# Kernel tuning notes

Hardware: AMD Instinct MI355X
Metric: run time of the kernel (lower is better)

## Reference

```python
import jax, jax.numpy as jnp
import numpy as np

R = 128          # voxel grid resolution
B = 2            # batch size
NPB = 250_000    # active voxels per batch item
N = B * NPB      # total active voxels
C_IN = 32        # in_nchannel
C0 = 32          # enc_ch[0] = out_nchannel
C1 = 32          # enc_ch[1]
EPS = 1e-5


def _build_neighbor_maps():
    """Build Minkowski-style kernel maps: for each kernel offset k and output
    voxel n, nmap[k, n] = index of the input voxel at coord+offset, or -1."""
    rng = np.random.default_rng(0)
    keys_list = []
    for b in range(B):
        flat = rng.choice(R ** 3, NPB, replace=False).astype(np.int64)
        keys_list.append(b * (R ** 3) + np.sort(flat))
    keys = np.concatenate(keys_list)  # globally sorted (batch-major)
    local = keys % (R ** 3)
    bidx = keys // (R ** 3)
    x = local // (R * R)
    y = (local // R) % R
    z = local % R

    def make(offsets):
        nmap = np.full((len(offsets), N), -1, dtype=np.int32)
        for k, (dx, dy, dz) in enumerate(offsets):
            nx, ny, nz = x + dx, y + dy, z + dz
            valid = (nx >= 0) & (nx < R) & (ny >= 0) & (ny < R) & (nz >= 0) & (nz < R)
            nkey = bidx * (R ** 3) + nx * R * R + ny * R + nz
            pos = np.searchsorted(keys, nkey)
            pos_c = np.clip(pos, 0, N - 1)
            valid &= keys[pos_c] == nkey
            nmap[k] = np.where(valid, pos_c, -1)
        return nmap

    off3 = [(dx, dy, dz) for dx in (-1, 0, 1) for dy in (-1, 0, 1) for dz in (-1, 0, 1)]
    off2 = [(dx, dy, dz) for dx in (0, 1) for dy in (0, 1) for dz in (0, 1)]
    return jnp.asarray(make(off3)), jnp.asarray(make(off2))


def setup_inputs() -> dict:
    key = jax.random.key(0)
    ks = jax.random.split(key, 8)
    nmap3, nmap2 = _build_neighbor_maps()
    s3_in = 1.0 / np.sqrt(27 * C_IN)
    s2 = 1.0 / np.sqrt(8 * C0)
    s3 = 1.0 / np.sqrt(27 * C1)
    return {
        "feats": jax.random.normal(ks[0], (N, C_IN), jnp.float32),
        "W1": jax.random.normal(ks[1], (27, C_IN, C0), jnp.float32) * s3_in,
        "g1": jnp.ones((C0,), jnp.float32),
        "b1": jnp.zeros((C0,), jnp.float32),
        "W2": jax.random.normal(ks[2], (8, C0, C1), jnp.float32) * s2,
        "g2": jnp.ones((C1,), jnp.float32),
        "b2": jnp.zeros((C1,), jnp.float32),
        "W3": jax.random.normal(ks[3], (27, C1, C1), jnp.float32) * s3,
        "g3": jnp.ones((C1,), jnp.float32),
        "b3": jnp.zeros((C1,), jnp.float32),
        "nmap3": nmap3,
        "nmap2": nmap2,
    }


def sparse_conv(feats, nmap, W):
    """MinkowskiConvolution (no bias): gather neighbors per kernel offset,
    GEMM with that offset's weight, accumulate. Loop is over the fixed,
    small kernel volume (8 or 27), not over data."""
    out = jnp.zeros((feats.shape[0], W.shape[-1]), feats.dtype)
    for k in range(W.shape[0]):
        idx = nmap[k]
        g = jnp.where((idx >= 0)[:, None], feats[jnp.maximum(idx, 0)], 0.0)
        out = out + g @ W[k]
    return out


def bn_elu(x, gamma, beta):
    # MinkowskiBatchNorm over all active voxels (training-mode stats) + ELU
    mean = jnp.mean(x, axis=0)
    var = jnp.var(x, axis=0)
    xn = (x - mean) * jax.lax.rsqrt(var + EPS)
    return jax.nn.elu(xn * gamma + beta)


def reference(feats, W1, g1, b1, W2, g2, b2, W3, g3, b3, nmap3, nmap2):
    # enc_block_s1: conv k=3 s=1 -> BN -> ELU
    h = bn_elu(sparse_conv(feats, nmap3, W1), g1, b1)
    # enc_block_s1s2: conv k=2 s=1 -> BN -> ELU -> conv k=3 -> BN -> ELU
    h = bn_elu(sparse_conv(h, nmap2, W2), g2, b2)
    h = bn_elu(sparse_conv(h, nmap3, W3), g3, b3)
    return h
```

## Files before the change

### kernel.cpp

```cpp
#include <hip/hip_runtime.h>


typedef short shortx8 __attribute__((ext_vector_type(8)));
typedef float floatx4 __attribute__((ext_vector_type(4)));

__device__ __forceinline__ float bf2f(unsigned short h) {
    unsigned u = ((unsigned)h) << 16;
    return __builtin_bit_cast(float, u);
}
__device__ __forceinline__ unsigned short f2bf(float f) {
    unsigned u = __builtin_bit_cast(unsigned, f);
    return (unsigned short)((u + 0x7fffu + ((u >> 16) & 1u)) >> 16);
}

__device__ __forceinline__ void gl_lds16(const void* g, void* l) {
    __builtin_amdgcn_global_load_lds(
        (const __attribute__((address_space(1))) unsigned*)g,
        (__attribute__((address_space(3))) unsigned*)l, 16, 0, 0);
}

__global__ void detect_dtype(const unsigned* __restrict__ g1, int* __restrict__ flag) {
    if (threadIdx.x == 0) *flag = (g1[0] == 0x3F800000u) ? 1 : 0;
}

__global__ __launch_bounds__(256) void prep_w_all(
    const void* __restrict__ W1_, const void* __restrict__ W2_,
    const void* __restrict__ W3_, unsigned short* __restrict__ Wg,
    const int* __restrict__ flag)
{
    int o = blockIdx.x * 256 + threadIdx.x;
    if (o >= 62 * 1024) return;
    const void* W; int lo;
    if (o < 27648)      { W = W1_; lo = o; }
    else if (o < 35840) { W = W2_; lo = o - 27648; }
    else                { W = W3_; lo = o - 35840; }
    int j = lo & 7, lane = (lo >> 3) & 63, f = (lo >> 9) & 1, k = lo >> 10;
    int col = lane & 15, quad = lane >> 4;
    int src = k * 1024 + (quad * 8 + j) * 32 + f * 16 + col;
    unsigned short v = *flag ? f2bf(((const float*)W)[src])
                             : ((const unsigned short*)W)[src];
    Wg[o] = v;
}

__global__ __launch_bounds__(256) void normalize_feats(
    const void* __restrict__ in_, unsigned short* __restrict__ out,
    int total, const int* __restrict__ flag)
{
    if (!*flag) return;
    int i = (blockIdx.x * 256 + threadIdx.x) * 8;
    if (i >= total) return;
    const float* in = (const float*)in_;
    floatx4 a = *(const floatx4*)(in + i);
    floatx4 b = *(const floatx4*)(in + i + 4);
    unsigned o[4];
    o[0] = (unsigned)f2bf(a[0]) | ((unsigned)f2bf(a[1]) << 16);
    o[1] = (unsigned)f2bf(a[2]) | ((unsigned)f2bf(a[3]) << 16);
    o[2] = (unsigned)f2bf(b[0]) | ((unsigned)f2bf(b[1]) << 16);
    o[3] = (unsigned)f2bf(b[2]) | ((unsigned)f2bf(b[3]) << 16);
    uint4 ov = {o[0], o[1], o[2], o[3]};
    *(uint4*)(out + i) = ov;
}

template <int KV>
__global__ __launch_bounds__(512, 4) void conv_stats(
    const unsigned short* __restrict__ feats,
    const unsigned short* __restrict__ feats_alt,
    const unsigned short* __restrict__ Wg,
    const int* __restrict__ nmap,
    unsigned short* __restrict__ xout,
    float* __restrict__ stat,
    int N,
    const int* __restrict__ flagA)
{
    constexpr int CH  = (KV >= 9) ? 9 : KV;
    constexpr int NCH = KV / CH;
    static_assert(KV % CH == 0, "chunking assumes CH | KV");
    constexpr int BUFB = CH * 4096;

    __shared__ __align__(16) char smem[2 * BUFB + 2048];
    float* red = (float*)(smem + 2 * BUFB);

    const int tid  = threadIdx.x;
    const int lane = tid & 63, wave = tid >> 6;
    const int col  = lane & 15, quad = lane >> 4;
    const int row0 = blockIdx.x * 512;
    const int m0   = row0 + wave * 64;
    const unsigned short* A = (*flagA) ? feats_alt : feats;

    auto stage = [&](int c) {
        const int kc = c * CH;
        char* buf = smem + (c & 1) * BUFB;
        for (int s = wave; s < CH * 4; s += 8) {
            int ki = s >> 2, part = s & 3;
            if (part < 2) {
                int r4 = row0 + part * 256 + lane * 4;
                if (r4 > N - 4) r4 = N - 4;
                gl_lds16(nmap + (size_t)(kc + ki) * N + r4,
                         buf + ki * 2048 + part * 1024);
            } else {
                gl_lds16(Wg + (kc + ki) * 1024 + (part - 2) * 512 + lane * 8,
                         buf + CH * 2048 + ki * 2048 + (part - 2) * 1024);
            }
        }
    };

    floatx4 accA[4], accB[4];
#pragma unroll
    for (int t = 0; t < 4; ++t) {
        accA[t] = {0.f, 0.f, 0.f, 0.f};
        accB[t] = {0.f, 0.f, 0.f, 0.f};
    }

    int rown[4];
#pragma unroll
    for (int t = 0; t < 4; ++t) rown[t] = m0 + t * 16 + col;

    stage(0);
    __syncthreads();

    for (int c = 0; c < NCH; ++c) {
        if (c + 1 < NCH) stage(c + 1);
        const int* nsl = (const int*)(smem + (c & 1) * BUFB);
        const unsigned short* wsl =
            (const unsigned short*)(smem + (c & 1) * BUFB + CH * 2048);

        shortx8 ring[2][4];
#pragma unroll
        for (int p = 0; p < 2; ++p) {
#pragma unroll
            for (int t = 0; t < 4; ++t) {
                int id = (rown[t] < N) ? nsl[p * 512 + wave * 64 + t * 16 + col] : -1;
                shortx8 a = {0, 0, 0, 0, 0, 0, 0, 0};
                if (id >= 0) a = *(const shortx8*)(A + (size_t)id * 32 + quad * 8);
                ring[p][t] = a;
            }
        }

#pragma unroll
        for (int kk = 0; kk < CH; ++kk) {
            shortx8 at[4];
#pragma unroll
            for (int t = 0; t < 4; ++t) at[t] = ring[kk & 1][t];

            if (kk + 2 < CH) {
#pragma unroll
                for (int t = 0; t < 4; ++t) {
                    int id = (rown[t] < N)
                                 ? nsl[(kk + 2) * 512 + wave * 64 + t * 16 + col]
                                 : -1;
                    shortx8 a = {0, 0, 0, 0, 0, 0, 0, 0};
                    if (id >= 0) a = *(const shortx8*)(A + (size_t)id * 32 + quad * 8);
                    ring[kk & 1][t] = a;
                }
            }

            shortx8 b0 = *(const shortx8*)(wsl + kk * 1024 + lane * 8);
            shortx8 b1 = *(const shortx8*)(wsl + kk * 1024 + 512 + lane * 8);
#pragma unroll
            for (int t = 0; t < 4; ++t) {
                accA[t] = __builtin_amdgcn_mfma_f32_16x16x32_bf16(at[t], b0, accA[t], 0, 0, 0);
                accB[t] = __builtin_amdgcn_mfma_f32_16x16x32_bf16(at[t], b1, accB[t], 0, 0, 0);
            }
            __builtin_amdgcn_sched_barrier(0);
        }
        __syncthreads();
    }

#pragma unroll
    for (int t = 0; t < 4; ++t) {
        int rbase = m0 + t * 16 + quad * 4;
#pragma unroll
        for (int r = 0; r < 4; ++r) {
            int row = rbase + r;
            if (row < N) {
                xout[row * 32 + col]      = f2bf(accA[t][r]);
                xout[row * 32 + col + 16] = f2bf(accB[t][r]);
            }
        }
    }

    float s0 = 0.f, s1 = 0.f, q0 = 0.f, q1 = 0.f;
#pragma unroll
    for (int t = 0; t < 4; ++t) {
#pragma unroll
        for (int r = 0; r < 4; ++r) {
            s0 += accA[t][r]; q0 += accA[t][r] * accA[t][r];
            s1 += accB[t][r]; q1 += accB[t][r] * accB[t][r];
        }
    }
    s0 += __shfl_xor(s0, 16); s0 += __shfl_xor(s0, 32);
    s1 += __shfl_xor(s1, 16); s1 += __shfl_xor(s1, 32);
    q0 += __shfl_xor(q0, 16); q0 += __shfl_xor(q0, 32);
    q1 += __shfl_xor(q1, 16); q1 += __shfl_xor(q1, 32);

    if (lane < 16) {
        float* rw = red + wave * 64;
        rw[col]      = s0;
        rw[col + 16] = s1;
        rw[col + 32] = q0;
        rw[col + 48] = q1;
    }
    __syncthreads();
    if (tid < 64) {
        float v = 0.f;
#pragma unroll
        for (int w = 0; w < 8; ++w) v += red[tid + w * 64];
        atomicAdd(stat + tid, v);
    }
}

__global__ __launch_bounds__(256) void bn_elu_apply(
    const unsigned short* __restrict__ x,
    const float* __restrict__ stat,
    const void* __restrict__ g_,
    const void* __restrict__ b_,
    void* __restrict__ out_,
    int total, int N, int finalout,
    const int* __restrict__ flag)
{
    __shared__ float ps[64];
    int tid = threadIdx.x;
    if (tid < 32) {
        int f = *flag;
        float gv = f ? ((const float*)g_)[tid] : bf2f(((const unsigned short*)g_)[tid]);
        float bv = f ? ((const float*)b_)[tid] : bf2f(((const unsigned short*)b_)[tid]);
        float invN = 1.0f / (float)N;
        float mean = stat[tid] * invN;
        float var  = fmaxf(stat[32 + tid] * invN - mean * mean, 0.0f);
        float sc   = gv * rsqrtf(var + 1e-5f);
        ps[tid]      = sc;
        ps[32 + tid] = bv - mean * sc;
    }
    __syncthreads();

    int i = (blockIdx.x * 256 + tid) * 8;
    if (i >= total) return;

    uint4 v = *(const uint4*)(x + i);
    int c0 = i & 31;
    unsigned w[4] = {v.x, v.y, v.z, v.w};
    float y[8];
#pragma unroll
    for (int j = 0; j < 4; ++j) {
        int c = c0 + 2 * j;
        float f0 = bf2f((unsigned short)(w[j] & 0xffffu));
        float f1 = bf2f((unsigned short)(w[j] >> 16));
        float y0 = f0 * ps[c]     + ps[32 + c];
        float y1 = f1 * ps[c + 1] + ps[32 + c + 1];
        y[2*j]     = y0 > 0.f ? y0 : (__expf(y0) - 1.f);
        y[2*j + 1] = y1 > 0.f ? y1 : (__expf(y1) - 1.f);
    }

    if (finalout && *flag) {
        float* o = (float*)out_ + i;
        floatx4 o0 = {y[0], y[1], y[2], y[3]};
        floatx4 o1 = {y[4], y[5], y[6], y[7]};
        *(floatx4*)o = o0;
        *(floatx4*)(o + 4) = o1;
    } else {
        unsigned o[4];
#pragma unroll
        for (int j = 0; j < 4; ++j)
            o[j] = (unsigned)f2bf(y[2*j]) | ((unsigned)f2bf(y[2*j + 1]) << 16);
        uint4 ov = {o[0], o[1], o[2], o[3]};
        *(uint4*)((unsigned short*)out_ + i) = ov;
    }
}

extern "C" void kernel_launch(void* const* d_in, const int* in_sizes, int n_in,
                              void* d_out, int out_size, void* d_ws, size_t ws_size,
                              hipStream_t stream)
{
    const void* feats = d_in[0];
    const void* W1    = d_in[1];
    const void* g1    = d_in[2];
    const void* b1    = d_in[3];
    const void* W2    = d_in[4];
    const void* g2    = d_in[5];
    const void* b2    = d_in[6];
    const void* W3    = d_in[7];
    const void* g3    = d_in[8];
    const void* b3    = d_in[9];
    const int* nmap3  = (const int*)d_in[10];
    const int* nmap2  = (const int*)d_in[11];

    const int N = in_sizes[0] / 32;
    const int total = N * 32;

    char* ws = (char*)d_ws;
    float* stat0 = (float*)(ws);
    float* stat1 = (float*)(ws + 256);
    float* stat2 = (float*)(ws + 512);
    int*   flagD = (int*)(ws + 768);
    unsigned short* Wg  = (unsigned short*)(ws + 4096);
    unsigned short* Wg1 = Wg;
    unsigned short* Wg2 = Wg + 27648;
    unsigned short* Wg3 = Wg + 35840;
    unsigned short* xbuf = (unsigned short*)(ws + 131072);
    unsigned short* hbuf = (unsigned short*)d_out;

    hipMemsetAsync(d_ws, 0, 1024, stream);
    detect_dtype<<<1, 64, 0, stream>>>((const unsigned*)g1, flagD);

    prep_w_all<<<(62 * 1024 + 255) / 256, 256, 0, stream>>>(W1, W2, W3, Wg, flagD);
    normalize_feats<<<(total / 8 + 255) / 256, 256, 0, stream>>>(feats, hbuf, total, flagD);

    const int cblocks = (N + 511) / 512;
    const int ablocks = (total / 8 + 255) / 256;

    conv_stats<27><<<cblocks, 512, 0, stream>>>(
        (const unsigned short*)feats, hbuf, Wg1, nmap3, xbuf, stat0, N, flagD);
    bn_elu_apply<<<ablocks, 256, 0, stream>>>(xbuf, stat0, g1, b1, hbuf, total, N, 0, flagD);

    conv_stats<8><<<cblocks, 512, 0, stream>>>(
        hbuf, hbuf, Wg2, nmap2, xbuf, stat1, N, flagD);
    bn_elu_apply<<<ablocks, 256, 0, stream>>>(xbuf, stat1, g2, b2, hbuf, total, N, 0, flagD);

    conv_stats<27><<<cblocks, 512, 0, stream>>>(
        hbuf, hbuf, Wg3, nmap3, xbuf, stat2, N, flagD);
    bn_elu_apply<<<ablocks, 256, 0, stream>>>(xbuf, stat2, g3, b3, d_out, total, N, 1, flagD);
}
```

Before: 354.4 us.

## Prefetch neighbor indices into registers and stage all weights in LDS once

The chunked double-buffered LDS staging of neighbor-map indices and weights is removed. Each thread now loads its own nmap indices straight from global memory with nontemporal loads, four offsets ahead, and gathers features three offsets deep into a register ring. All KV weight slices are copied to LDS once up front, so the per-chunk syncthreads go away. Invalid neighbors read from a zeroed row in workspace instead of taking a branch. This uses more registers for the deeper prefetch queues, which may lower occupancy.

After: 377.1 us. +6.4%, slower.

```diff
diff --git a/kernel.cpp b/kernel.cpp
--- a/kernel.cpp
+++ b/kernel.cpp
@@ -67,42 +67,29 @@
     const unsigned short* __restrict__ feats_alt,
     const unsigned short* __restrict__ Wg,
     const int* __restrict__ nmap,
+    const unsigned short* __restrict__ zrow,
     unsigned short* __restrict__ xout,
     float* __restrict__ stat,
     int N,
     const int* __restrict__ flagA)
 {
-    constexpr int CH  = (KV >= 9) ? 9 : KV;
-    constexpr int NCH = KV / CH;
-    static_assert(KV % CH == 0, "chunking assumes CH | KV");
-    constexpr int BUFB = CH * 4096;
-
-    __shared__ __align__(16) char smem[2 * BUFB + 2048];
-    float* red = (float*)(smem + 2 * BUFB);
+    __shared__ __align__(16) char smem[KV * 2048 + 2048];
+    float* red = (float*)(smem + KV * 2048);
 
     const int tid  = threadIdx.x;
     const int lane = tid & 63, wave = tid >> 6;
     const int col  = lane & 15, quad = lane >> 4;
-    const int row0 = blockIdx.x * 512;
-    const int m0   = row0 + wave * 64;
+    const int m0   = blockIdx.x * 512 + wave * 64;
     const unsigned short* A = (*flagA) ? feats_alt : feats;
 
-    auto stage = [&](int c) {
-        const int kc = c * CH;
-        char* buf = smem + (c & 1) * BUFB;
-        for (int s = wave; s < CH * 4; s += 8) {
-            int ki = s >> 2, part = s & 3;
-            if (part < 2) {
-                int r4 = row0 + part * 256 + lane * 4;
-                if (r4 > N - 4) r4 = N - 4;
-                gl_lds16(nmap + (size_t)(kc + ki) * N + r4,
-                         buf + ki * 2048 + part * 1024);
-            } else {
-                gl_lds16(Wg + (kc + ki) * 1024 + (part - 2) * 512 + lane * 8,
-                         buf + CH * 2048 + ki * 2048 + (part - 2) * 1024);
-            }
-        }
-    };
+    int rown[4], rcl[4];
+    bool ok[4];
+#pragma unroll
+    for (int t = 0; t < 4; ++t) {
+        rown[t] = m0 + t * 16 + col;
+        ok[t]   = rown[t] < N;
+        rcl[t]  = ok[t] ? rown[t] : (N - 1);
+    }
 
     floatx4 accA[4], accB[4];
 #pragma unroll
@@ -111,59 +98,45 @@
         accB[t] = {0.f, 0.f, 0.f, 0.f};
     }
 
-    int rown[4];
-#pragma unroll
-    for (int t = 0; t < 4; ++t) rown[t] = m0 + t * 16 + col;
-
-    stage(0);
+    int idxq[4][4];
+    shortx8 ring[3][4];
+
+    auto IDX = [&](int k) {
+#pragma unroll
+        for (int t = 0; t < 4; ++t) {
+            int id = __builtin_nontemporal_load(nmap + (size_t)k * N + rcl[t]);
+            idxq[k & 3][t] = ok[t] ? id : -1;
+        }
+    };
+    auto GAT = [&](int k) {
+#pragma unroll
+        for (int t = 0; t < 4; ++t) {
+            int id = idxq[k & 3][t];
+            const unsigned short* src = (id >= 0) ? (A + (size_t)id * 32) : zrow;
+            ring[k % 3][t] = *(const shortx8*)(src + quad * 8);
+        }
+    };
+
+    IDX(0); IDX(1); IDX(2); IDX(3);
+    for (int s = wave; s < KV * 2; s += 8)
+        gl_lds16(Wg + s * 512 + lane * 8, smem + s * 1024);
+    GAT(0); GAT(1);
     __syncthreads();
 
-    for (int c = 0; c < NCH; ++c) {
-        if (c + 1 < NCH) stage(c + 1);
-        const int* nsl = (const int*)(smem + (c & 1) * BUFB);
-        const unsigned short* wsl =
-            (const unsigned short*)(smem + (c & 1) * BUFB + CH * 2048);
-
-        shortx8 ring[2][4];
-#pragma unroll
-        for (int p = 0; p < 2; ++p) {
-#pragma unroll
-            for (int t = 0; t < 4; ++t) {
-                int id = (rown[t] < N) ? nsl[p * 512 + wave * 64 + t * 16 + col] : -1;
-                shortx8 a = {0, 0, 0, 0, 0, 0, 0, 0};
-                if (id >= 0) a = *(const shortx8*)(A + (size_t)id * 32 + quad * 8);
-                ring[p][t] = a;
-            }
-        }
-
-#pragma unroll
-        for (int kk = 0; kk < CH; ++kk) {
-            shortx8 at[4];
-#pragma unroll
-            for (int t = 0; t < 4; ++t) at[t] = ring[kk & 1][t];
-
-            if (kk + 2 < CH) {
-#pragma unroll
-                for (int t = 0; t < 4; ++t) {
-                    int id = (rown[t] < N)
-                                 ? nsl[(kk + 2) * 512 + wave * 64 + t * 16 + col]
-                                 : -1;
-                    shortx8 a = {0, 0, 0, 0, 0, 0, 0, 0};
-                    if (id >= 0) a = *(const shortx8*)(A + (size_t)id * 32 + quad * 8);
-                    ring[kk & 1][t] = a;
-                }
-            }
-
-            shortx8 b0 = *(const shortx8*)(wsl + kk * 1024 + lane * 8);
-            shortx8 b1 = *(const shortx8*)(wsl + kk * 1024 + 512 + lane * 8);
-#pragma unroll
-            for (int t = 0; t < 4; ++t) {
-                accA[t] = __builtin_amdgcn_mfma_f32_16x16x32_bf16(at[t], b0, accA[t], 0, 0, 0);
-                accB[t] = __builtin_amdgcn_mfma_f32_16x16x32_bf16(at[t], b1, accB[t], 0, 0, 0);
-            }
-            __builtin_amdgcn_sched_barrier(0);
-        }
-        __syncthreads();
+#pragma unroll
+    for (int k = 0; k < KV; ++k) {
+        if (k + 4 < KV) IDX(k + 4);
+        if (k + 2 < KV) GAT(k + 2);
+
+        const unsigned short* wk = (const unsigned short*)(smem + k * 2048);
+        shortx8 b0 = *(const shortx8*)(wk + lane * 8);
+        shortx8 b1 = *(const shortx8*)(wk + 512 + lane * 8);
+#pragma unroll
+        for (int t = 0; t < 4; ++t) {
+            accA[t] = __builtin_amdgcn_mfma_f32_16x16x32_bf16(ring[k % 3][t], b0, accA[t], 0, 0, 0);
+            accB[t] = __builtin_amdgcn_mfma_f32_16x16x32_bf16(ring[k % 3][t], b1, accB[t], 0, 0, 0);
+        }
+        __builtin_amdgcn_sched_barrier(0);
     }
 
 #pragma unroll
@@ -292,6 +265,7 @@
     float* stat1 = (float*)(ws + 256);
     float* stat2 = (float*)(ws + 512);
     int*   flagD = (int*)(ws + 768);
+    const unsigned short* zrow = (const unsigned short*)(ws + 1024);
     unsigned short* Wg  = (unsigned short*)(ws + 4096);
     unsigned short* Wg1 = Wg;
     unsigned short* Wg2 = Wg + 27648;
@@ -299,7 +273,7 @@
     unsigned short* xbuf = (unsigned short*)(ws + 131072);
     unsigned short* hbuf = (unsigned short*)d_out;
 
-    hipMemsetAsync(d_ws, 0, 1024, stream);
+    hipMemsetAsync(d_ws, 0, 2048, stream);
     detect_dtype<<<1, 64, 0, stream>>>((const unsigned*)g1, flagD);
 
     prep_w_all<<<(62 * 1024 + 255) / 256, 256, 0, stream>>>(W1, W2, W3, Wg, flagD);
@@ -309,14 +283,14 @@
     const int ablocks = (total / 8 + 255) / 256;
 
     conv_stats<27><<<cblocks, 512, 0, stream>>>(
-        (const unsigned short*)feats, hbuf, Wg1, nmap3, xbuf, stat0, N, flagD);
+        (const unsigned short*)feats, hbuf, Wg1, nmap3, zrow, xbuf, stat0, N, flagD);
     bn_elu_apply<<<ablocks, 256, 0, stream>>>(xbuf, stat0, g1, b1, hbuf, total, N, 0, flagD);
 
     conv_stats<8><<<cblocks, 512, 0, stream>>>(
-        hbuf, hbuf, Wg2, nmap2, xbuf, stat1, N, flagD);
+        hbuf, hbuf, Wg2, nmap2, zrow, xbuf, stat1, N, flagD);
     bn_elu_apply<<<ablocks, 256, 0, stream>>>(xbuf, stat1, g2, b2, hbuf, total, N, 0, flagD);
 
     conv_stats<27><<<cblocks, 512, 0, stream>>>(
-        hbuf, hbuf, Wg3, nmap3, xbuf, stat2, N, flagD);
+        hbuf, hbuf, Wg3, nmap3, zrow, xbuf, stat2, N, flagD);
     bn_elu_apply<<<ablocks, 256, 0, stream>>>(xbuf, stat2, g3, b3, d_out, total, N, 1, flagD);
 }
```

## Fuse all stages into one persistent kernel with software grid barriers

Applied to the files above, without the earlier changes.

Replaces the nine separate launches (dtype detect, weight prep, feature conversion, three conv+stats and three BN+ELU passes) with a single persistent kernel of 512 blocks. Phases are separated by an atomic-counter grid barrier, and each phase loops over tiles or elements with a grid stride. This removes launch gaps and inter-kernel idle time. In exchange, the fixed grid size may lower occupancy during the gather-heavy conv phases and adds barrier spin cost. It also relies on all blocks being co-resident.

Result: slower. 1.071 ms (+202.3%).

```diff
diff --git a/kernel.cpp b/kernel.cpp
--- a/kernel.cpp
+++ b/kernel.cpp
@@ -3,6 +3,9 @@
 
 typedef short shortx8 __attribute__((ext_vector_type(8)));
 typedef float floatx4 __attribute__((ext_vector_type(4)));
+
+constexpr int GRID_B = 512;
+constexpr int TPB    = 512;
 
 __device__ __forceinline__ float bf2f(unsigned short h) {
     unsigned u = ((unsigned)h) << 16;
@@ -19,252 +22,275 @@
         (__attribute__((address_space(3))) unsigned*)l, 16, 0, 0);
 }
 
-__global__ void detect_dtype(const unsigned* __restrict__ g1, int* __restrict__ flag) {
-    if (threadIdx.x == 0) *flag = (g1[0] == 0x3F800000u) ? 1 : 0;
-}
-
-__global__ __launch_bounds__(256) void prep_w_all(
-    const void* __restrict__ W1_, const void* __restrict__ W2_,
-    const void* __restrict__ W3_, unsigned short* __restrict__ Wg,
-    const int* __restrict__ flag)
-{
-    int o = blockIdx.x * 256 + threadIdx.x;
-    if (o >= 62 * 1024) return;
-    const void* W; int lo;
-    if (o < 27648)      { W = W1_; lo = o; }
-    else if (o < 35840) { W = W2_; lo = o - 27648; }
-    else                { W = W3_; lo = o - 35840; }
-    int j = lo & 7, lane = (lo >> 3) & 63, f = (lo >> 9) & 1, k = lo >> 10;
-    int col = lane & 15, quad = lane >> 4;
-    int src = k * 1024 + (quad * 8 + j) * 32 + f * 16 + col;
-    unsigned short v = *flag ? f2bf(((const float*)W)[src])
-                             : ((const unsigned short*)W)[src];
-    Wg[o] = v;
-}
-
-__global__ __launch_bounds__(256) void normalize_feats(
-    const void* __restrict__ in_, unsigned short* __restrict__ out,
-    int total, const int* __restrict__ flag)
-{
-    if (!*flag) return;
-    int i = (blockIdx.x * 256 + threadIdx.x) * 8;
-    if (i >= total) return;
-    const float* in = (const float*)in_;
-    floatx4 a = *(const floatx4*)(in + i);
-    floatx4 b = *(const floatx4*)(in + i + 4);
-    unsigned o[4];
-    o[0] = (unsigned)f2bf(a[0]) | ((unsigned)f2bf(a[1]) << 16);
-    o[1] = (unsigned)f2bf(a[2]) | ((unsigned)f2bf(a[3]) << 16);
-    o[2] = (unsigned)f2bf(b[0]) | ((unsigned)f2bf(b[1]) << 16);
-    o[3] = (unsigned)f2bf(b[2]) | ((unsigned)f2bf(b[3]) << 16);
-    uint4 ov = {o[0], o[1], o[2], o[3]};
-    *(uint4*)(out + i) = ov;
+__device__ __forceinline__ void gridbar(unsigned* cnt, unsigned* gen) {
+    __syncthreads();
+    if (threadIdx.x == 0) {
+        __threadfence();
+        unsigned g = __hip_atomic_load(gen, __ATOMIC_RELAXED, __HIP_MEMORY_SCOPE_AGENT);
+        unsigned a = __hip_atomic_fetch_add(cnt, 1u, __ATOMIC_ACQ_REL, __HIP_MEMORY_SCOPE_AGENT);
+        if (a == GRID_B - 1) {
+            __hip_atomic_store(cnt, 0u, __ATOMIC_RELAXED, __HIP_MEMORY_SCOPE_AGENT);
+            __hip_atomic_store(gen, g + 1u, __ATOMIC_RELEASE, __HIP_MEMORY_SCOPE_AGENT);
+        } else {
+            while (__hip_atomic_load(gen, __ATOMIC_ACQUIRE, __HIP_MEMORY_SCOPE_AGENT) == g)
+                __builtin_amdgcn_s_sleep(8);
+        }
+        __threadfence();
+    }
+    __syncthreads();
 }
 
 template <int KV>
-__global__ __launch_bounds__(512, 4) void conv_stats(
-    const unsigned short* __restrict__ feats,
-    const unsigned short* __restrict__ feats_alt,
-    const unsigned short* __restrict__ Wg,
-    const int* __restrict__ nmap,
-    unsigned short* __restrict__ xout,
-    float* __restrict__ stat,
-    int N,
-    const int* __restrict__ flagA)
+__device__ void conv_phase(char* smem,
+    const unsigned short* A, const unsigned short* Wg,
+    const int* nmap, unsigned short* xout, float* stat,
+    int N, int ntiles)
 {
     constexpr int CH  = (KV >= 9) ? 9 : KV;
     constexpr int NCH = KV / CH;
-    static_assert(KV % CH == 0, "chunking assumes CH | KV");
     constexpr int BUFB = CH * 4096;
-
-    __shared__ __align__(16) char smem[2 * BUFB + 2048];
     float* red = (float*)(smem + 2 * BUFB);
 
     const int tid  = threadIdx.x;
     const int lane = tid & 63, wave = tid >> 6;
     const int col  = lane & 15, quad = lane >> 4;
-    const int row0 = blockIdx.x * 512;
-    const int m0   = row0 + wave * 64;
-    const unsigned short* A = (*flagA) ? feats_alt : feats;
-
-    auto stage = [&](int c) {
-        const int kc = c * CH;
-        char* buf = smem + (c & 1) * BUFB;
-        for (int s = wave; s < CH * 4; s += 8) {
-            int ki = s >> 2, part = s & 3;
-            if (part < 2) {
-                int r4 = row0 + part * 256 + lane * 4;
-                if (r4 > N - 4) r4 = N - 4;
-                gl_lds16(nmap + (size_t)(kc + ki) * N + r4,
-                         buf + ki * 2048 + part * 1024);
-            } else {
-                gl_lds16(Wg + (kc + ki) * 1024 + (part - 2) * 512 + lane * 8,
-                         buf + CH * 2048 + ki * 2048 + (part - 2) * 1024);
-            }
-        }
-    };
-
-    floatx4 accA[4], accB[4];
-#pragma unroll
-    for (int t = 0; t < 4; ++t) {
-        accA[t] = {0.f, 0.f, 0.f, 0.f};
-        accB[t] = {0.f, 0.f, 0.f, 0.f};
-    }
-
-    int rown[4];
-#pragma unroll
-    for (int t = 0; t < 4; ++t) rown[t] = m0 + t * 16 + col;
-
-    stage(0);
-    __syncthreads();
-
-    for (int c = 0; c < NCH; ++c) {
-        if (c + 1 < NCH) stage(c + 1);
-        const int* nsl = (const int*)(smem + (c & 1) * BUFB);
-        const unsigned short* wsl =
-            (const unsigned short*)(smem + (c & 1) * BUFB + CH * 2048);
-
-        shortx8 ring[2][4];
-#pragma unroll
-        for (int p = 0; p < 2; ++p) {
-#pragma unroll
-            for (int t = 0; t < 4; ++t) {
-                int id = (rown[t] < N) ? nsl[p * 512 + wave * 64 + t * 16 + col] : -1;
-                shortx8 a = {0, 0, 0, 0, 0, 0, 0, 0};
-                if (id >= 0) a = *(const shortx8*)(A + (size_t)id * 32 + quad * 8);
-                ring[p][t] = a;
-            }
-        }
-
-#pragma unroll
-        for (int kk = 0; kk < CH; ++kk) {
-            shortx8 at[4];
-#pragma unroll
-            for (int t = 0; t < 4; ++t) at[t] = ring[kk & 1][t];
-
-            if (kk + 2 < CH) {
+
+    for (int tile = blockIdx.x; tile < ntiles; tile += GRID_B) {
+        const int row0 = tile * 512;
+        const int m0   = row0 + wave * 64;
+
+        auto stage = [&](int c) {
+            const int kc = c * CH;
+            char* buf = smem + (c & 1) * BUFB;
+            for (int s = wave; s < CH * 4; s += 8) {
+                int ki = s >> 2, part = s & 3;
+                if (part < 2) {
+                    int r4 = row0 + part * 256 + lane * 4;
+                    if (r4 > N - 4) r4 = N - 4;
+                    gl_lds16(nmap + (size_t)(kc + ki) * N + r4,
+                             buf + ki * 2048 + part * 1024);
+                } else {
+                    gl_lds16(Wg + (kc + ki) * 1024 + (part - 2) * 512 + lane * 8,
+                             buf + CH * 2048 + ki * 2048 + (part - 2) * 1024);
+                }
+            }
+        };
+
+        floatx4 accA[4], accB[4];
+#pragma unroll
+        for (int t = 0; t < 4; ++t) {
+            accA[t] = {0.f, 0.f, 0.f, 0.f};
+            accB[t] = {0.f, 0.f, 0.f, 0.f};
+        }
+
+        int rown[4];
+#pragma unroll
+        for (int t = 0; t < 4; ++t) rown[t] = m0 + t * 16 + col;
+
+        stage(0);
+        __syncthreads();
+
+        for (int c = 0; c < NCH; ++c) {
+            if (c + 1 < NCH) stage(c + 1);
+            const int* nsl = (const int*)(smem + (c & 1) * BUFB);
+            const unsigned short* wsl =
+                (const unsigned short*)(smem + (c & 1) * BUFB + CH * 2048);
+
+            shortx8 ring[2][4];
+#pragma unroll
+            for (int p = 0; p < 2; ++p) {
 #pragma unroll
                 for (int t = 0; t < 4; ++t) {
-                    int id = (rown[t] < N)
-                                 ? nsl[(kk + 2) * 512 + wave * 64 + t * 16 + col]
-                                 : -1;
+                    int id = (rown[t] < N) ? nsl[p * 512 + wave * 64 + t * 16 + col] : -1;
                     shortx8 a = {0, 0, 0, 0, 0, 0, 0, 0};
                     if (id >= 0) a = *(const shortx8*)(A + (size_t)id * 32 + quad * 8);
-                    ring[kk & 1][t] = a;
-                }
-            }
-
-            shortx8 b0 = *(const shortx8*)(wsl + kk * 1024 + lane * 8);
-            shortx8 b1 = *(const shortx8*)(wsl + kk * 1024 + 512 + lane * 8);
-#pragma unroll
-            for (int t = 0; t < 4; ++t) {
-                accA[t] = __builtin_amdgcn_mfma_f32_16x16x32_bf16(at[t], b0, accA[t], 0, 0, 0);
-                accB[t] = __builtin_amdgcn_mfma_f32_16x16x32_bf16(at[t], b1, accB[t], 0, 0, 0);
-            }
-            __builtin_amdgcn_sched_barrier(0);
+                    ring[p][t] = a;
+                }
+            }
+
+#pragma unroll
+            for (int kk = 0; kk < CH; ++kk) {
+                shortx8 at[4];
+#pragma unroll
+                for (int t = 0; t < 4; ++t) at[t] = ring[kk & 1][t];
+
+                if (kk + 2 < CH) {
+#pragma unroll
+                    for (int t = 0; t < 4; ++t) {
+                        int id = (rown[t] < N)
+                                     ? nsl[(kk + 2) * 512 + wave * 64 + t * 16 + col]
+                                     : -1;
+                        shortx8 a = {0, 0, 0, 0, 0, 0, 0, 0};
+                        if (id >= 0) a = *(const shortx8*)(A + (size_t)id * 32 + quad * 8);
+                        ring[kk & 1][t] = a;
+                    }
+                }
+
+                shortx8 b0 = *(const shortx8*)(wsl + kk * 1024 + lane * 8);
+                shortx8 b1 = *(const shortx8*)(wsl + kk * 1024 + 512 + lane * 8);
+#pragma unroll
+                for (int t = 0; t < 4; ++t) {
+                    accA[t] = __builtin_amdgcn_mfma_f32_16x16x32_bf16(at[t], b0, accA[t], 0, 0, 0);
+                    accB[t] = __builtin_amdgcn_mfma_f32_16x16x32_bf16(at[t], b1, accB[t], 0, 0, 0);
+                }
+                __builtin_amdgcn_sched_barrier(0);
+            }
+            __syncthreads();
+        }
+
+#pragma unroll
+        for (int t = 0; t < 4; ++t) {
+            int rbase = m0 + t * 16 + quad * 4;
+#pragma unroll
+            for (int r = 0; r < 4; ++r) {
+                int row = rbase + r;
+                if (row < N) {
+                    xout[row * 32 + col]      = f2bf(accA[t][r]);
+                    xout[row * 32 + col + 16] = f2bf(accB[t][r]);
+                }
+            }
+        }
+
+        float s0 = 0.f, s1 = 0.f, q0 = 0.f, q1 = 0.f;
+#pragma unroll
+        for (int t = 0; t < 4; ++t) {
+#pragma unroll
+            for (int r = 0; r < 4; ++r) {
+                s0 += accA[t][r]; q0 += accA[t][r] * accA[t][r];
+                s1 += accB[t][r]; q1 += accB[t][r] * accB[t][r];
+            }
+        }
+        s0 += __shfl_xor(s0, 16); s0 += __shfl_xor(s0, 32);
+        s1 += __shfl_xor(s1, 16); s1 += __shfl_xor(s1, 32);
+        q0 += __shfl_xor(q0, 16); q0 += __shfl_xor(q0, 32);
+        q1 += __shfl_xor(q1, 16); q1 += __shfl_xor(q1, 32);
+
+        if (lane < 16) {
+            float* rw = red + wave * 64;
+            rw[col]      = s0;
+            rw[col + 16] = s1;
+            rw[col + 32] = q0;
+            rw[col + 48] = q1;
         }
         __syncthreads();
-    }
-
-#pragma unroll
-    for (int t = 0; t < 4; ++t) {
-        int rbase = m0 + t * 16 + quad * 4;
-#pragma unroll
-        for (int r = 0; r < 4; ++r) {
-            int row = rbase + r;
-            if (row < N) {
-                xout[row * 32 + col]      = f2bf(accA[t][r]);
-                xout[row * 32 + col + 16] = f2bf(accB[t][r]);
-            }
-        }
-    }
-
-    float s0 = 0.f, s1 = 0.f, q0 = 0.f, q1 = 0.f;
-#pragma unroll
-    for (int t = 0; t < 4; ++t) {
-#pragma unroll
-        for (int r = 0; r < 4; ++r) {
-            s0 += accA[t][r]; q0 += accA[t][r] * accA[t][r];
-            s1 += accB[t][r]; q1 += accB[t][r] * accB[t][r];
-        }
-    }
-    s0 += __shfl_xor(s0, 16); s0 += __shfl_xor(s0, 32);
-    s1 += __shfl_xor(s1, 16); s1 += __shfl_xor(s1, 32);
-    q0 += __shfl_xor(q0, 16); q0 += __shfl_xor(q0, 32);
-    q1 += __shfl_xor(q1, 16); q1 += __shfl_xor(q1, 32);
-
-    if (lane < 16) {
-        float* rw = red + wave * 64;
-        rw[col]      = s0;
-        rw[col + 16] = s1;
-        rw[col + 32] = q0;
-        rw[col + 48] = q1;
-    }
-    __syncthreads();
-    if (tid < 64) {
-        float v = 0.f;
-#pragma unroll
-        for (int w = 0; w < 8; ++w) v += red[tid + w * 64];
-        atomicAdd(stat + tid, v);
-    }
-}
-
-__global__ __launch_bounds__(256) void bn_elu_apply(
-    const unsigned short* __restrict__ x,
-    const float* __restrict__ stat,
-    const void* __restrict__ g_,
-    const void* __restrict__ b_,
-    void* __restrict__ out_,
-    int total, int N, int finalout,
-    const int* __restrict__ flag)
+        if (tid < 64) {
+            float v = 0.f;
+#pragma unroll
+            for (int w = 0; w < 8; ++w) v += red[tid + w * 64];
+            atomicAdd(stat + tid, v);
+        }
+    }
+}
+
+__device__ void bn_phase(char* smem,
+    const unsigned short* x, float* stat,
+    const void* g_, const void* b_, void* out_,
+    int total, int N, int finalout, int flag)
 {
-    __shared__ float ps[64];
-    int tid = threadIdx.x;
+    float* ps = (float*)smem;
+    const int tid = threadIdx.x;
     if (tid < 32) {
-        int f = *flag;
-        float gv = f ? ((const float*)g_)[tid] : bf2f(((const unsigned short*)g_)[tid]);
-        float bv = f ? ((const float*)b_)[tid] : bf2f(((const unsigned short*)b_)[tid]);
+        float gv = flag ? ((const float*)g_)[tid] : bf2f(((const unsigned short*)g_)[tid]);
+        float bv = flag ? ((const float*)b_)[tid] : bf2f(((const unsigned short*)b_)[tid]);
+        float s  = __hip_atomic_load(stat + tid,      __ATOMIC_RELAXED, __HIP_MEMORY_SCOPE_AGENT);
+        float sq = __hip_atomic_load(stat + 32 + tid, __ATOMIC_RELAXED, __HIP_MEMORY_SCOPE_AGENT);
         float invN = 1.0f / (float)N;
-        float mean = stat[tid] * invN;
-        float var  = fmaxf(stat[32 + tid] * invN - mean * mean, 0.0f);
+        float mean = s * invN;
+        float var  = fmaxf(sq * invN - mean * mean, 0.0f);
         float sc   = gv * rsqrtf(var + 1e-5f);
         ps[tid]      = sc;
         ps[32 + tid] = bv - mean * sc;
     }
     __syncthreads();
 
-    int i = (blockIdx.x * 256 + tid) * 8;
-    if (i >= total) return;
-
-    uint4 v = *(const uint4*)(x + i);
-    int c0 = i & 31;
-    unsigned w[4] = {v.x, v.y, v.z, v.w};
-    float y[8];
-#pragma unroll
-    for (int j = 0; j < 4; ++j) {
-        int c = c0 + 2 * j;
-        float f0 = bf2f((unsigned short)(w[j] & 0xffffu));
-        float f1 = bf2f((unsigned short)(w[j] >> 16));
-        float y0 = f0 * ps[c]     + ps[32 + c];
-        float y1 = f1 * ps[c + 1] + ps[32 + c + 1];
-        y[2*j]     = y0 > 0.f ? y0 : (__expf(y0) - 1.f);
-        y[2*j + 1] = y1 > 0.f ? y1 : (__expf(y1) - 1.f);
-    }
-
-    if (finalout && *flag) {
-        float* o = (float*)out_ + i;
-        floatx4 o0 = {y[0], y[1], y[2], y[3]};
-        floatx4 o1 = {y[4], y[5], y[6], y[7]};
-        *(floatx4*)o = o0;
-        *(floatx4*)(o + 4) = o1;
-    } else {
-        unsigned o[4];
-#pragma unroll
-        for (int j = 0; j < 4; ++j)
-            o[j] = (unsigned)f2bf(y[2*j]) | ((unsigned)f2bf(y[2*j + 1]) << 16);
-        uint4 ov = {o[0], o[1], o[2], o[3]};
-        *(uint4*)((unsigned short*)out_ + i) = ov;
-    }
+    for (int i = (blockIdx.x * TPB + tid) * 8; i < total; i += GRID_B * TPB * 8) {
+        uint4 v = *(const uint4*)(x + i);
+        int c0 = i & 31;
+        unsigned w[4] = {v.x, v.y, v.z, v.w};
+        float y[8];
+#pragma unroll
+        for (int j = 0; j < 4; ++j) {
+            int c = c0 + 2 * j;
+            float f0 = bf2f((unsigned short)(w[j] & 0xffffu));
+            float f1 = bf2f((unsigned short)(w[j] >> 16));
+            float y0 = f0 * ps[c]     + ps[32 + c];
+            float y1 = f1 * ps[c + 1] + ps[32 + c + 1];
+            y[2*j]     = y0 > 0.f ? y0 : (__expf(y0) - 1.f);
+            y[2*j + 1] = y1 > 0.f ? y1 : (__expf(y1) - 1.f);
+        }
+        if (finalout && flag) {
+            float* o = (float*)out_ + i;
+            floatx4 o0 = {y[0], y[1], y[2], y[3]};
+            floatx4 o1 = {y[4], y[5], y[6], y[7]};
+            *(floatx4*)o = o0;
+            *(floatx4*)(o + 4) = o1;
+        } else {
+            unsigned o[4];
+#pragma unroll
+            for (int j = 0; j < 4; ++j)
+                o[j] = (unsigned)f2bf(y[2*j]) | ((unsigned)f2bf(y[2*j + 1]) << 16);
+            uint4 ov = {o[0], o[1], o[2], o[3]};
+            *(uint4*)((unsigned short*)out_ + i) = ov;
+        }
+    }
+}
+
+__global__ __launch_bounds__(512, 4) void fused_net(
+    const unsigned short* feats_b, const void* feats_raw,
+    const void* W1_, const void* g1_, const void* b1_,
+    const void* W2_, const void* g2_, const void* b2_,
+    const void* W3_, const void* g3_, const void* b3_,
+    const int* nmap3, const int* nmap2,
+    unsigned short* Wg, unsigned short* xbuf, unsigned short* hbuf,
+    float* stat0, float* stat1, float* stat2,
+    unsigned* cnt, unsigned* gen,
+    void* dout, int N, int total, int ntiles)
+{
+    __shared__ __align__(16) char smem[9 * 4096 * 2 + 2048];
+
+    const int tid  = threadIdx.x;
+    const int flag = (((const unsigned*)g1_)[0] == 0x3F800000u) ? 1 : 0;
+
+    for (int o = blockIdx.x * TPB + tid; o < 62 * 1024; o += GRID_B * TPB) {
+        const void* W; int lo;
+        if (o < 27648)      { W = W1_; lo = o; }
+        else if (o < 35840) { W = W2_; lo = o - 27648; }
+        else                { W = W3_; lo = o - 35840; }
+        int j = lo & 7, lane = (lo >> 3) & 63, f = (lo >> 9) & 1, k = lo >> 10;
+        int c = lane & 15, q = lane >> 4;
+        int src = k * 1024 + (q * 8 + j) * 32 + f * 16 + c;
+        Wg[o] = flag ? f2bf(((const float*)W)[src])
+                     : ((const unsigned short*)W)[src];
+    }
+    if (flag) {
+        const float* in = (const float*)feats_raw;
+        for (int i = (blockIdx.x * TPB + tid) * 8; i < total; i += GRID_B * TPB * 8) {
+            floatx4 a = *(const floatx4*)(in + i);
+            floatx4 b = *(const floatx4*)(in + i + 4);
+            unsigned o[4];
+            o[0] = (unsigned)f2bf(a[0]) | ((unsigned)f2bf(a[1]) << 16);
+            o[1] = (unsigned)f2bf(a[2]) | ((unsigned)f2bf(a[3]) << 16);
+            o[2] = (unsigned)f2bf(b[0]) | ((unsigned)f2bf(b[1]) << 16);
+            o[3] = (unsigned)f2bf(b[2]) | ((unsigned)f2bf(b[3]) << 16);
+            uint4 ov = {o[0], o[1], o[2], o[3]};
+            *(uint4*)(hbuf + i) = ov;
+        }
+    }
+    gridbar(cnt, gen);
+
+    conv_phase<27>(smem, flag ? hbuf : feats_b, Wg, nmap3, xbuf, stat0, N, ntiles);
+    gridbar(cnt, gen);
+    bn_phase(smem, xbuf, stat0, g1_, b1_, hbuf, total, N, 0, flag);
+    gridbar(cnt, gen);
+
+    conv_phase<8>(smem, hbuf, Wg + 27648, nmap2, xbuf, stat1, N, ntiles);
+    gridbar(cnt, gen);
+    bn_phase(smem, xbuf, stat1, g2_, b2_, hbuf, total, N, 0, flag);
+    gridbar(cnt, gen);
+
+    conv_phase<27>(smem, hbuf, Wg + 35840, nmap3, xbuf, stat2, N, ntiles);
+    gridbar(cnt, gen);
+    bn_phase(smem, xbuf, stat2, g3_, b3_, dout, total, N, 1, flag);
 }
 
 extern "C" void kernel_launch(void* const* d_in, const int* in_sizes, int n_in,
@@ -286,37 +312,26 @@
 
     const int N = in_sizes[0] / 32;
     const int total = N * 32;
+    const int ntiles = (N + 511) / 512;
 
     char* ws = (char*)d_ws;
-    float* stat0 = (float*)(ws);
-    float* stat1 = (float*)(ws + 256);
-    float* stat2 = (float*)(ws + 512);
-    int*   flagD = (int*)(ws + 768);
-    unsigned short* Wg  = (unsigned short*)(ws + 4096);
-    unsigned short* Wg1 = Wg;
-    unsigned short* Wg2 = Wg + 27648;
-    unsigned short* Wg3 = Wg + 35840;
+    float*    stat0 = (float*)(ws);
+    float*    stat1 = (float*)(ws + 256);
+    float*    stat2 = (float*)(ws + 512);
+    unsigned* cnt   = (unsigned*)(ws + 768);
+    unsigned* gen   = (unsigned*)(ws + 772);
+    unsigned short* Wg   = (unsigned short*)(ws + 4096);
     unsigned short* xbuf = (unsigned short*)(ws + 131072);
     unsigned short* hbuf = (unsigned short*)d_out;
 
     hipMemsetAsync(d_ws, 0, 1024, stream);
-    detect_dtype<<<1, 64, 0, stream>>>((const unsigned*)g1, flagD);
-
-    prep_w_all<<<(62 * 1024 + 255) / 256, 256, 0, stream>>>(W1, W2, W3, Wg, flagD);
-    normalize_feats<<<(total / 8 + 255) / 256, 256, 0, stream>>>(feats, hbuf, total, flagD);
-
-    const int cblocks = (N + 511) / 512;
-    const int ablocks = (total / 8 + 255) / 256;
-
-    conv_stats<27><<<cblocks, 512, 0, stream>>>(
-        (const unsigned short*)feats, hbuf, Wg1, nmap3, xbuf, stat0, N, flagD);
-    bn_elu_apply<<<ablocks, 256, 0, stream>>>(xbuf, stat0, g1, b1, hbuf, total, N, 0, flagD);
-
-    conv_stats<8><<<cblocks, 512, 0, stream>>>(
-        hbuf, hbuf, Wg2, nmap2, xbuf, stat1, N, flagD);
-    bn_elu_apply<<<ablocks, 256, 0, stream>>>(xbuf, stat1, g2, b2, hbuf, total, N, 0, flagD);
-
-    conv_stats<27><<<cblocks, 512, 0, stream>>>(
-        hbuf, hbuf, Wg3, nmap3, xbuf, stat2, N, flagD);
-    bn_elu_apply<<<ablocks, 256, 0, stream>>>(xbuf, stat2, g3, b3, d_out, total, N, 1, flagD);
-}
+
+    fused_net<<<GRID_B, TPB, 0, stream>>>(
+        (const unsigned short*)feats, feats,
+        W1, g1, b1, W2, g2, b2, W3, g3, b3,
+        nmap3, nmap2,
+        Wg, xbuf, hbuf,
+        stat0, stat1, stat2,
+        cnt, gen,
+        d_out, N, total, ntiles);
+}
```
